# Optimization experiments

Measured on AMD Instinct MI355X. Metric: run time of the kernel, lower is better.

The kernel has to match this reference:

```python
import jax, jax.numpy as jnp
import numpy as np
import math

B, S, D = 16, 512, 512
H = 8
RET = 512  # return_dim, multiple of D
EPS = 1e-12


def _xavier(key, shape):
    bound = math.sqrt(6.0 / (shape[0] + shape[1]))
    return jax.random.uniform(key, shape, jnp.float32, -bound, bound)


def setup_inputs() -> dict:
    key = jax.random.key(0)
    ks = jax.random.split(key, 7)
    x = jax.random.normal(ks[0], (B, S, D), jnp.float32)
    WQ = _xavier(ks[1], (D, D))
    WK = _xavier(ks[2], (D, D))
    WV = _xavier(ks[3], (D, D))
    # LazyLinear over flattened (S*D) features; stored [in, out] for clean matmul
    Wlin = jax.random.normal(ks[4], (S * D, RET), jnp.float32) / math.sqrt(S * D)
    blin = jnp.zeros((RET,), jnp.float32)
    ln_w = jnp.ones((D,), jnp.float32)
    ln_b = jnp.zeros((D,), jnp.float32)
    return {"x": x, "WQ": WQ, "WK": WK, "WV": WV,
            "Wlin": Wlin, "blin": blin, "ln_w": ln_w, "ln_b": ln_b}


def _swish(v):
    return v * jax.nn.sigmoid(v)


def reference(x, WQ, WK, WV, Wlin, blin, ln_w, ln_b):
    b, s, d = x.shape
    dh = d // H
    # QKV projections -> [b, h, s, dh]
    Q = (x @ WQ).reshape(b, s, H, dh).transpose(0, 2, 1, 3)
    K = (x @ WK).reshape(b, s, H, dh).transpose(0, 2, 1, 3)
    V = (x @ WV).reshape(b, s, H, dh).transpose(0, 2, 1, 3)
    # swish-gated attention scores (no softmax)
    scores = jnp.einsum('bhqd,bhkd->bhqk', Q, K) / math.sqrt(dh)
    scores = _swish(scores)
    out = jnp.einsum('bhqk,bhkd->bqhd', scores, V).reshape(b, s, d)
    # residual + TF-style LayerNorm (residual_coef = 1)
    out = out + x
    u = out.mean(-1, keepdims=True)
    var = jnp.mean((out - u) ** 2, axis=-1, keepdims=True)
    out = ln_w * ((out - u) / jnp.sqrt(var + EPS)) + ln_b
    # linear over flattened seq*d features, swish, reshape (dropout = identity, eval)
    y = out.reshape(b, -1) @ Wlin + blin
    y = _swish(y)
    return y.reshape(b, -1, d)
```

## Files before the change

kernel.cpp:

```cpp
#include <hip/hip_runtime.h>
#include <cstdint>

#define TB 16
#define TS 512
#define TD 512
#define TH 8
#define TDH 64
#define TSD (TS*TD)

typedef __attribute__((ext_vector_type(8))) short s16x8;
typedef __attribute__((ext_vector_type(4))) float f32x4;
typedef unsigned short bfu;

__device__ __forceinline__ unsigned short f2b(float f) {
  unsigned int u = __float_as_uint(f);
  u += 0x7FFFu + ((u >> 16) & 1u);
  return (unsigned short)(u >> 16);
}
__device__ __forceinline__ float b2f(bfu h) {
  return __uint_as_float(((unsigned)h) << 16);
}

__device__ __forceinline__ void gll16(const void* g, void* l) {
  __builtin_amdgcn_global_load_lds((const __attribute__((address_space(1))) void*)g,
                                   (__attribute__((address_space(3))) void*)l, 16, 0, 0);
}

__device__ __forceinline__ f32x4 MFMA16(s16x8 a, s16x8 b, f32x4 c) {
  return __builtin_amdgcn_mfma_f32_16x16x32_bf16(a, b, c, 0, 0, 0);
}

__global__ __launch_bounds__(256) void k_cast_x(const float4* __restrict__ x, ushort4* __restrict__ xb) {
  int i = blockIdx.x * 256 + threadIdx.x;
  float4 v = x[i];
  ushort4 o; o.x = f2b(v.x); o.y = f2b(v.y); o.z = f2b(v.z); o.w = f2b(v.w);
  xb[i] = o;
}

__global__ __launch_bounds__(256) void k_prep_w(const float* __restrict__ WQ, const float* __restrict__ WK,
                                                const float* __restrict__ WV, bfu* __restrict__ wt) {
  __shared__ float tile[64][65];
  int bk = blockIdx.x & 7;
  int bn = blockIdx.x >> 3;
  const float* W = bn < 8 ? WQ : (bn < 16 ? WK : WV);
  int ncol0 = (bn & 7) * 64;
  int t = threadIdx.x, tx = t & 63, ty = t >> 6;
  #pragma unroll
  for (int i = 0; i < 16; ++i) {
    int kl = i * 4 + ty;
    tile[kl][tx] = W[(size_t)(bk * 64 + kl) * 512 + ncol0 + tx];
  }
  __syncthreads();
  #pragma unroll
  for (int i = 0; i < 16; ++i) {
    int nl = i * 4 + ty;
    wt[(size_t)(bn * 64 + nl) * 512 + bk * 64 + tx] = f2b(tile[tx][nl]);
  }
}

__global__ __launch_bounds__(256) void k_qkv(const bfu* __restrict__ xb, const bfu* __restrict__ wt,
                                             bfu* __restrict__ qb, bfu* __restrict__ kb, bfu* __restrict__ vtb) {
  __shared__ __align__(16) bfu At[128 * 32];
  __shared__ __align__(16) bfu Bt[128 * 32];
  int t = threadIdx.x, lane = t & 63, w = t >> 6;
  int wr = w >> 1, wc = w & 1;
  int m0 = blockIdx.x * 128, n0 = blockIdx.y * 128;
  int fr = lane & 15, hi = lane >> 4;
  f32x4 acc[4][4] = {};
  for (int k0 = 0; k0 < TD; k0 += 32) {
    #pragma unroll
    for (int i = 0; i < 2; ++i) {
      int base = (i * 4 + w) * 1024;
      int seg  = (i * 4 + w) * 64 + lane;
      int row = seg >> 2, cs = seg & 3;
      gll16(xb + (size_t)(m0 + row) * TD + k0 + cs * 8, (char*)At + base);
      gll16(wt + (size_t)(n0 + row) * TD + k0 + cs * 8, (char*)Bt + base);
    }
    __syncthreads();
    s16x8 a[4], bb[4];
    #pragma unroll
    for (int m = 0; m < 4; ++m) a[m]  = *(const s16x8*)&At[(wr * 64 + m * 16 + fr) * 32 + hi * 8];
    #pragma unroll
    for (int n = 0; n < 4; ++n) bb[n] = *(const s16x8*)&Bt[(wc * 64 + n * 16 + fr) * 32 + hi * 8];
    #pragma unroll
    for (int m = 0; m < 4; ++m)
      #pragma unroll
      for (int n = 0; n < 4; ++n)
        acc[m][n] = MFMA16(a[m], bb[n], acc[m][n]);
    __syncthreads();
  }
  #pragma unroll
  for (int m = 0; m < 4; ++m) {
    int grow = m0 + wr * 64 + m * 16 + hi * 4;
    #pragma unroll
    for (int n = 0; n < 4; ++n) {
      int gcol = n0 + wc * 64 + n * 16 + fr;
      if (gcol < 512) {
        #pragma unroll
        for (int r = 0; r < 4; ++r) qb[(size_t)(grow + r) * TD + gcol] = f2b(acc[m][n][r]);
      } else if (gcol < 1024) {
        int c = gcol - 512;
        #pragma unroll
        for (int r = 0; r < 4; ++r) kb[(size_t)(grow + r) * TD + c] = f2b(acc[m][n][r]);
      } else {
        int c = gcol - 1024;
        int hh = c >> 6, dc = c & 63;
        int b_ = grow >> 9, s = grow & 511;
        ushort4 pk;
        pk.x = f2b(acc[m][n][0]); pk.y = f2b(acc[m][n][1]);
        pk.z = f2b(acc[m][n][2]); pk.w = f2b(acc[m][n][3]);
        *(ushort4*)&vtb[((size_t)((b_ * TH + hh) * TDH + dc) << 9) + s] = pk;
      }
    }
  }
}

__global__ __launch_bounds__(256) void k_attn(const bfu* __restrict__ qb, const bfu* __restrict__ kb,
                                              const bfu* __restrict__ vtb, const bfu* __restrict__ xb,
                                              float* __restrict__ ao) {
  __shared__ __align__(16) bfu Qs[64 * 72];
  __shared__ __align__(16) bfu Ks[128 * 72];
  __shared__ __align__(16) bfu Vs[64 * 136];
  __shared__ __align__(16) bfu Ps[64 * 136];
  int t = threadIdx.x, lane = t & 63, w = t >> 6;
  int qt = blockIdx.x, h = blockIdx.y, b = blockIdx.z;
  size_t qrow0 = (size_t)b * TS + qt * 64;
  int fr = lane & 15, hi = lane >> 4;
  #pragma unroll
  for (int i = 0; i < 2; ++i) {
    int seg = i * 256 + t, row = seg >> 3, cs = seg & 7;
    s16x8 v = *(const s16x8*)(qb + (qrow0 + row) * TD + h * TDH + cs * 8);
    *(s16x8*)&Qs[row * 72 + cs * 8] = v;
  }
  f32x4 acc_o[4] = {};
  for (int kt = 0; kt < 4; ++kt) {
    #pragma unroll
    for (int i = 0; i < 4; ++i) {
      int seg = i * 256 + t, row = seg >> 3, cs = seg & 7;
      s16x8 v = *(const s16x8*)(kb + ((size_t)b * TS + kt * 128 + row) * TD + h * TDH + cs * 8);
      *(s16x8*)&Ks[row * 72 + cs * 8] = v;
    }
    #pragma unroll
    for (int i = 0; i < 4; ++i) {
      int seg = i * 256 + t, row = seg >> 4, cs = seg & 15;
      s16x8 v = *(const s16x8*)(vtb + ((size_t)(b * TH + h) * TDH + row) * TS + kt * 128 + cs * 8);
      *(s16x8*)&Vs[row * 136 + cs * 8] = v;
    }
    __syncthreads();
    s16x8 aq0 = *(const s16x8*)&Qs[(w * 16 + fr) * 72 + hi * 8];
    s16x8 aq1 = *(const s16x8*)&Qs[(w * 16 + fr) * 72 + 32 + hi * 8];
    f32x4 sc[8];
    #pragma unroll
    for (int kj = 0; kj < 8; ++kj) {
      s16x8 b0 = *(const s16x8*)&Ks[(kj * 16 + fr) * 72 + hi * 8];
      s16x8 b1 = *(const s16x8*)&Ks[(kj * 16 + fr) * 72 + 32 + hi * 8];
      f32x4 c = {};
      c = MFMA16(aq0, b0, c);
      c = MFMA16(aq1, b1, c);
      sc[kj] = c;
    }
    #pragma unroll
    for (int kj = 0; kj < 8; ++kj) {
      #pragma unroll
      for (int r = 0; r < 4; ++r) {
        float v = sc[kj][r] * 0.125f;
        float p = v / (1.f + __expf(-v));
        Ps[(w * 16 + hi * 4 + r) * 136 + kj * 16 + fr] = f2b(p);
      }
    }
    #pragma unroll
    for (int ks = 0; ks < 4; ++ks) {
      s16x8 pa = *(const s16x8*)&Ps[(w * 16 + fr) * 136 + ks * 32 + hi * 8];
      #pragma unroll
      for (int dn = 0; dn < 4; ++dn) {
        s16x8 vb = *(const s16x8*)&Vs[(dn * 16 + fr) * 136 + ks * 32 + hi * 8];
        acc_o[dn] = MFMA16(pa, vb, acc_o[dn]);
      }
    }
    __syncthreads();
  }
  #pragma unroll
  for (int dn = 0; dn < 4; ++dn) {
    int col = h * TDH + dn * 16 + fr;
    #pragma unroll
    for (int r = 0; r < 4; ++r) {
      size_t row = qrow0 + w * 16 + hi * 4 + r;
      ao[row * TD + col] = acc_o[dn][r] + b2f(xb[row * TD + col]);
    }
  }
}

__global__ __launch_bounds__(256) void k_ln(const float* __restrict__ a, const float* __restrict__ w,
                                            const float* __restrict__ bias, bfu* __restrict__ o) {
  int row = blockIdx.x, t = threadIdx.x;
  float2 v = *(const float2*)(a + (size_t)row * TD + t * 2);
  float s = v.x + v.y;
  #pragma unroll
  for (int off = 32; off > 0; off >>= 1) s += __shfl_down(s, off);
  __shared__ float r1[4], r2[4];
  int lane = t & 63, wv = t >> 6;
  if (lane == 0) r1[wv] = s;
  __syncthreads();
  float mean = (r1[0] + r1[1] + r1[2] + r1[3]) * (1.f / TD);
  float dx = v.x - mean, dy = v.y - mean;
  float q = dx * dx + dy * dy;
  #pragma unroll
  for (int off = 32; off > 0; off >>= 1) q += __shfl_down(q, off);
  if (lane == 0) r2[wv] = q;
  __syncthreads();
  float var = (r2[0] + r2[1] + r2[2] + r2[3]) * (1.f / TD);
  float inv = rsqrtf(var + 1e-12f);
  float2 wv2 = *(const float2*)(w + t * 2);
  float2 bv2 = *(const float2*)(bias + t * 2);
  unsigned pack = (unsigned)f2b(wv2.x * dx * inv + bv2.x) |
                  ((unsigned)f2b(wv2.y * dy * inv + bv2.y) << 16);
  *(unsigned*)(o + (size_t)row * TD + t * 2) = pack;
}

__global__ __launch_bounds__(256) void k_lin_mfma(const bfu* __restrict__ lno, const float* __restrict__ wl,
                                                  float* __restrict__ part) {
  __shared__ __align__(16) bfu Wt[64 * 72];
  int t = threadIdx.x, lane = t & 63, w = t >> 6;
  int fr = lane & 15, hi = lane >> 4;
  int kc = blockIdx.x >> 3, nb = blockIdx.x & 7;
  int n0 = nb * 64;
  int nl = t & 63, kb = (t >> 6) * 16;
  int ks0 = kc * 2048;
  const float* wbase = wl + (size_t)(ks0 + kb) * 512 + n0 + nl;
  const bfu*   abase = lno + (size_t)fr * TSD + ks0 + hi * 8;
  f32x4 acc = {};
  float wA[16], wB[16];
  s16x8 aA0, aA1, aB0, aB1;
  #pragma unroll
  for (int i = 0; i < 16; ++i) wA[i] = __builtin_nontemporal_load(wbase + (size_t)i * 512);
  aA0 = *(const s16x8*)abase;
  aA1 = *(const s16x8*)(abase + 32);

#define LIN_STEP(CW, CA0, CA1, NW, NA0, NA1, S)                                   \
  { if (S) __syncthreads();                                                       \
    unsigned pk[8];                                                               \
    _Pragma("unroll")                                                             \
    for (int i = 0; i < 8; ++i)                                                   \
      pk[i] = (unsigned)f2b(CW[2*i]) | ((unsigned)f2b(CW[2*i+1]) << 16);          \
    *(uint4*)&Wt[nl * 72 + kb]     = *(uint4*)&pk[0];                             \
    *(uint4*)&Wt[nl * 72 + kb + 8] = *(uint4*)&pk[4];                             \
    if ((S) + 1 < 32) {                                                           \
      const float* wp2 = wbase + (size_t)((S) + 1) * 64 * 512;                    \
      _Pragma("unroll")                                                           \
      for (int i = 0; i < 16; ++i) NW[i] = __builtin_nontemporal_load(wp2 + (size_t)i * 512); \
      const bfu* ap2 = abase + ((S) + 1) * 64;                                    \
      NA0 = *(const s16x8*)ap2; NA1 = *(const s16x8*)(ap2 + 32);                  \
    }                                                                             \
    __syncthreads();                                                              \
    s16x8 b0 = *(const s16x8*)&Wt[(w * 16 + fr) * 72 + hi * 8];                   \
    s16x8 b1 = *(const s16x8*)&Wt[(w * 16 + fr) * 72 + 32 + hi * 8];              \
    acc = MFMA16(CA0, b0, acc);                                                   \
    acc = MFMA16(CA1, b1, acc); }

  for (int s = 0; s < 32; s += 2) {
    LIN_STEP(wA, aA0, aA1, wB, aB0, aB1, s)
    LIN_STEP(wB, aB0, aB1, wA, aA0, aA1, s + 1)
  }
#undef LIN_STEP
  #pragma unroll
  for (int r = 0; r < 4; ++r)
    part[(size_t)kc * 8192 + (hi * 4 + r) * 512 + n0 + w * 16 + fr] = acc[r];
}

__global__ __launch_bounds__(256) void k_lin_red(const float* __restrict__ part, const float* __restrict__ blin,
                                                 float* __restrict__ out) {
  int o = blockIdx.x * 256 + threadIdx.x;
  float s = 0.f;
  #pragma unroll 16
  for (int c = 0; c < 128; ++c) s += part[(size_t)c * 8192 + o];
  float v = s + blin[o & 511];
  out[o] = v / (1.f + __expf(-v));
}

extern "C" void kernel_launch(void* const* d_in, const int* in_sizes, int n_in,
                              void* d_out, int out_size, void* d_ws, size_t ws_size,
                              hipStream_t stream) {
  const float* x   = (const float*)d_in[0];
  const float* WQ  = (const float*)d_in[1];
  const float* WK  = (const float*)d_in[2];
  const float* WV  = (const float*)d_in[3];
  const float* Wl  = (const float*)d_in[4];
  const float* bl  = (const float*)d_in[5];
  const float* lnw = (const float*)d_in[6];
  const float* lnb = (const float*)d_in[7];
  float* out = (float*)d_out;
  char* ws = (char*)d_ws;
  bfu* xb  = (bfu*)ws;
  bfu* wt  = xb + 4194304;
  bfu* qb  = wt + 786432;
  bfu* kb  = qb + 4194304;
  bfu* vtb = kb + 4194304;
  float* attn = (float*)(vtb + 4194304);
  bfu*   lno  = (bfu*)(attn + 4194304);
  float* part = (float*)(lno + 4194304);
  float* pend = part + 1048576;
  (void)pend; (void)ws_size;

  k_cast_x  <<<4096, 256, 0, stream>>>((const float4*)x, (ushort4*)xb);
  k_prep_w  <<<192, 256, 0, stream>>>(WQ, WK, WV, wt);
  k_qkv     <<<dim3(64, 12), 256, 0, stream>>>(xb, wt, qb, kb, vtb);
  k_attn    <<<dim3(8, 8, 16), 256, 0, stream>>>(qb, kb, vtb, xb, attn);
  k_ln      <<<8192, 256, 0, stream>>>(attn, lnw, lnb, lno);
  k_lin_mfma<<<1024, 256, 0, stream>>>(lno, Wl, part);
  k_lin_red <<<32, 256, 0, stream>>>(part, bl, out);
}
```

Before: 198.9 us.

## Double-buffer QKV GEMM, XOR-swizzle LDS tiles, async-load attention, merge prep kernels

Merges the x-cast and weight-transpose kernels into one launch to save a kernel launch. The QKV GEMM gets double-buffered LDS with direct global-to-LDS loads, so the next K slice loads while MFMAs run. XOR-swizzled LDS layouts replace the padded ones in both GEMM and attention to avoid bank conflicts. Attention now uses global_load_lds for Q/K/V instead of going through registers. These changes add more index arithmetic and extra barriers in attention, and the swizzle indices must match exactly on write and read.

```diff
diff --git a/kernel.cpp b/kernel.cpp
--- a/kernel.cpp
+++ b/kernel.cpp
@@ -30,21 +30,24 @@
   return __builtin_amdgcn_mfma_f32_16x16x32_bf16(a, b, c, 0, 0, 0);
 }
 
-__global__ __launch_bounds__(256) void k_cast_x(const float4* __restrict__ x, ushort4* __restrict__ xb) {
-  int i = blockIdx.x * 256 + threadIdx.x;
-  float4 v = x[i];
-  ushort4 o; o.x = f2b(v.x); o.y = f2b(v.y); o.z = f2b(v.z); o.w = f2b(v.w);
-  xb[i] = o;
-}
-
-__global__ __launch_bounds__(256) void k_prep_w(const float* __restrict__ WQ, const float* __restrict__ WK,
-                                                const float* __restrict__ WV, bfu* __restrict__ wt) {
+__global__ __launch_bounds__(256) void k_prep(const float* __restrict__ x, ushort4* __restrict__ xb,
+                                              const float* __restrict__ WQ, const float* __restrict__ WK,
+                                              const float* __restrict__ WV, bfu* __restrict__ wt) {
+  int t = threadIdx.x;
+  if (blockIdx.x < 4096) {
+    int i = blockIdx.x * 256 + t;
+    float4 v = ((const float4*)x)[i];
+    ushort4 o; o.x = f2b(v.x); o.y = f2b(v.y); o.z = f2b(v.z); o.w = f2b(v.w);
+    xb[i] = o;
+    return;
+  }
   __shared__ float tile[64][65];
-  int bk = blockIdx.x & 7;
-  int bn = blockIdx.x >> 3;
+  int bid = blockIdx.x - 4096;
+  int bk = bid & 7;
+  int bn = bid >> 3;
   const float* W = bn < 8 ? WQ : (bn < 16 ? WK : WV);
   int ncol0 = (bn & 7) * 64;
-  int t = threadIdx.x, tx = t & 63, ty = t >> 6;
+  int tx = t & 63, ty = t >> 6;
   #pragma unroll
   for (int i = 0; i < 16; ++i) {
     int kl = i * 4 + ty;
@@ -60,35 +63,48 @@
 
 __global__ __launch_bounds__(256) void k_qkv(const bfu* __restrict__ xb, const bfu* __restrict__ wt,
                                              bfu* __restrict__ qb, bfu* __restrict__ kb, bfu* __restrict__ vtb) {
-  __shared__ __align__(16) bfu At[128 * 32];
-  __shared__ __align__(16) bfu Bt[128 * 32];
+  __shared__ __align__(16) bfu At[2][128 * 32];
+  __shared__ __align__(16) bfu Bt[2][128 * 32];
   int t = threadIdx.x, lane = t & 63, w = t >> 6;
   int wr = w >> 1, wc = w & 1;
   int m0 = blockIdx.x * 128, n0 = blockIdx.y * 128;
   int fr = lane & 15, hi = lane >> 4;
+  int l4r = lane >> 2, l4c = lane & 3;
   f32x4 acc[4][4] = {};
-  for (int k0 = 0; k0 < TD; k0 += 32) {
-    #pragma unroll
-    for (int i = 0; i < 2; ++i) {
-      int base = (i * 4 + w) * 1024;
-      int seg  = (i * 4 + w) * 64 + lane;
-      int row = seg >> 2, cs = seg & 3;
-      gll16(xb + (size_t)(m0 + row) * TD + k0 + cs * 8, (char*)At + base);
-      gll16(wt + (size_t)(n0 + row) * TD + k0 + cs * 8, (char*)Bt + base);
-    }
+
+#define QKV_STAGE(BUF, K0) { \
+    _Pragma("unroll") \
+    for (int i = 0; i < 2; ++i) { \
+      int row = i * 64 + w * 16 + l4r; \
+      int cs = l4c ^ (l4r & 3);                         \
+      gll16(xb + (size_t)(m0 + row) * TD + (K0) + cs * 8, (char*)At[BUF] + (i * 256 + w * 64) * 16); \
+      gll16(wt + (size_t)(n0 + row) * TD + (K0) + cs * 8, (char*)Bt[BUF] + (i * 256 + w * 64) * 16); \
+    } }
+
+#define QKV_COMP(BUF) { \
+    s16x8 a[4], bb[4]; \
+    int ca = (hi ^ (fr & 3)) * 8; \
+    _Pragma("unroll") \
+    for (int m = 0; m < 4; ++m) a[m]  = *(const s16x8*)&At[BUF][(wr * 64 + m * 16 + fr) * 32 + ca]; \
+    _Pragma("unroll") \
+    for (int n = 0; n < 4; ++n) bb[n] = *(const s16x8*)&Bt[BUF][(wc * 64 + n * 16 + fr) * 32 + ca]; \
+    _Pragma("unroll") \
+    for (int m = 0; m < 4; ++m) \
+      _Pragma("unroll") \
+      for (int n = 0; n < 4; ++n) \
+        acc[m][n] = MFMA16(a[m], bb[n], acc[m][n]); }
+
+  QKV_STAGE(0, 0)
+  __syncthreads();
+  for (int k = 0; k < 16; ++k) {
+    int cur = k & 1;
+    if (k < 15) QKV_STAGE(cur ^ 1, (k + 1) * 32)
+    QKV_COMP(cur)
     __syncthreads();
-    s16x8 a[4], bb[4];
-    #pragma unroll
-    for (int m = 0; m < 4; ++m) a[m]  = *(const s16x8*)&At[(wr * 64 + m * 16 + fr) * 32 + hi * 8];
-    #pragma unroll
-    for (int n = 0; n < 4; ++n) bb[n] = *(const s16x8*)&Bt[(wc * 64 + n * 16 + fr) * 32 + hi * 8];
-    #pragma unroll
-    for (int m = 0; m < 4; ++m)
-      #pragma unroll
-      for (int n = 0; n < 4; ++n)
-        acc[m][n] = MFMA16(a[m], bb[n], acc[m][n]);
-    __syncthreads();
-  }
+  }
+#undef QKV_STAGE
+#undef QKV_COMP
+
   #pragma unroll
   for (int m = 0; m < 4; ++m) {
     int grow = m0 + wr * 64 + m * 16 + hi * 4;
@@ -118,42 +134,56 @@
 __global__ __launch_bounds__(256) void k_attn(const bfu* __restrict__ qb, const bfu* __restrict__ kb,
                                               const bfu* __restrict__ vtb, const bfu* __restrict__ xb,
                                               float* __restrict__ ao) {
-  __shared__ __align__(16) bfu Qs[64 * 72];
-  __shared__ __align__(16) bfu Ks[128 * 72];
-  __shared__ __align__(16) bfu Vs[64 * 136];
-  __shared__ __align__(16) bfu Ps[64 * 136];
+  __shared__ __align__(16) bfu Qs[64 * 64];
+  __shared__ __align__(16) bfu Ks[128 * 64];
+  __shared__ __align__(16) bfu Vs[64 * 128];
+  __shared__ __align__(16) bfu Ps[64 * 128];
   int t = threadIdx.x, lane = t & 63, w = t >> 6;
   int qt = blockIdx.x, h = blockIdx.y, b = blockIdx.z;
   size_t qrow0 = (size_t)b * TS + qt * 64;
   int fr = lane & 15, hi = lane >> 4;
+  int l8r = lane >> 3, l8c = lane & 7;
+  int l16r = lane >> 4, l16c = lane & 15;
+
+#define K_STAGE(KT) { \
+    _Pragma("unroll") \
+    for (int i = 0; i < 4; ++i) { \
+      int row = i * 32 + w * 8 + l8r; \
+      int cs = l8c ^ (l8r & 7);                         \
+      gll16(kb + ((size_t)b * TS + (KT) * 128 + row) * TD + h * TDH + cs * 8, \
+            (char*)Ks + (i * 256 + w * 64) * 16); \
+    } }
+#define V_STAGE(KT) { \
+    _Pragma("unroll") \
+    for (int i = 0; i < 4; ++i) { \
+      int row = i * 16 + w * 4 + l16r; \
+      int cs = l16c ^ (row & 7); \
+      gll16(vtb + ((size_t)(b * TH + h) * TDH + row) * TS + (KT) * 128 + cs * 8, \
+            (char*)Vs + (i * 256 + w * 64) * 16); \
+    } }
+
   #pragma unroll
   for (int i = 0; i < 2; ++i) {
-    int seg = i * 256 + t, row = seg >> 3, cs = seg & 7;
-    s16x8 v = *(const s16x8*)(qb + (qrow0 + row) * TD + h * TDH + cs * 8);
-    *(s16x8*)&Qs[row * 72 + cs * 8] = v;
-  }
+    int row = i * 32 + w * 8 + l8r;
+    int cs = l8c ^ (l8r & 7);
+    gll16(qb + (qrow0 + row) * TD + h * TDH + cs * 8, (char*)Qs + (i * 256 + w * 64) * 16);
+  }
+  K_STAGE(0)
+  V_STAGE(0)
+  __syncthreads();
+
+  int qrow = w * 16 + fr;
+  int r7 = fr & 7;
   f32x4 acc_o[4] = {};
   for (int kt = 0; kt < 4; ++kt) {
-    #pragma unroll
-    for (int i = 0; i < 4; ++i) {
-      int seg = i * 256 + t, row = seg >> 3, cs = seg & 7;
-      s16x8 v = *(const s16x8*)(kb + ((size_t)b * TS + kt * 128 + row) * TD + h * TDH + cs * 8);
-      *(s16x8*)&Ks[row * 72 + cs * 8] = v;
-    }
-    #pragma unroll
-    for (int i = 0; i < 4; ++i) {
-      int seg = i * 256 + t, row = seg >> 4, cs = seg & 15;
-      s16x8 v = *(const s16x8*)(vtb + ((size_t)(b * TH + h) * TDH + row) * TS + kt * 128 + cs * 8);
-      *(s16x8*)&Vs[row * 136 + cs * 8] = v;
-    }
-    __syncthreads();
-    s16x8 aq0 = *(const s16x8*)&Qs[(w * 16 + fr) * 72 + hi * 8];
-    s16x8 aq1 = *(const s16x8*)&Qs[(w * 16 + fr) * 72 + 32 + hi * 8];
+    s16x8 aq0 = *(const s16x8*)&Qs[qrow * 64 + ((hi ^ r7) * 8)];
+    s16x8 aq1 = *(const s16x8*)&Qs[qrow * 64 + (((4 + hi) ^ r7) * 8)];
     f32x4 sc[8];
     #pragma unroll
     for (int kj = 0; kj < 8; ++kj) {
-      s16x8 b0 = *(const s16x8*)&Ks[(kj * 16 + fr) * 72 + hi * 8];
-      s16x8 b1 = *(const s16x8*)&Ks[(kj * 16 + fr) * 72 + 32 + hi * 8];
+      int krow = kj * 16 + fr;
+      s16x8 b0 = *(const s16x8*)&Ks[krow * 64 + ((hi ^ r7) * 8)];
+      s16x8 b1 = *(const s16x8*)&Ks[krow * 64 + (((4 + hi) ^ r7) * 8)];
       f32x4 c = {};
       c = MFMA16(aq0, b0, c);
       c = MFMA16(aq1, b1, c);
@@ -165,20 +195,29 @@
       for (int r = 0; r < 4; ++r) {
         float v = sc[kj][r] * 0.125f;
         float p = v / (1.f + __expf(-v));
-        Ps[(w * 16 + hi * 4 + r) * 136 + kj * 16 + fr] = f2b(p);
+        int prow = w * 16 + hi * 4 + r;
+        int c8 = (kj * 2 + (fr >> 3)) ^ (prow & 7);
+        Ps[prow * 128 + c8 * 8 + (fr & 7)] = f2b(p);
       }
     }
     #pragma unroll
     for (int ks = 0; ks < 4; ++ks) {
-      s16x8 pa = *(const s16x8*)&Ps[(w * 16 + fr) * 136 + ks * 32 + hi * 8];
+      s16x8 pa = *(const s16x8*)&Ps[qrow * 128 + (((ks * 4 + hi) ^ r7) * 8)];
       #pragma unroll
       for (int dn = 0; dn < 4; ++dn) {
-        s16x8 vb = *(const s16x8*)&Vs[(dn * 16 + fr) * 136 + ks * 32 + hi * 8];
+        s16x8 vb = *(const s16x8*)&Vs[(dn * 16 + fr) * 128 + (((ks * 4 + hi) ^ r7) * 8)];
         acc_o[dn] = MFMA16(pa, vb, acc_o[dn]);
       }
     }
     __syncthreads();
-  }
+    if (kt < 3) {
+      K_STAGE(kt + 1)
+      V_STAGE(kt + 1)
+      __syncthreads();
+    }
+  }
+#undef K_STAGE
+#undef V_STAGE
   #pragma unroll
   for (int dn = 0; dn < 4; ++dn) {
     int col = h * TDH + dn * 16 + fr;
@@ -298,11 +337,8 @@
   float* attn = (float*)(vtb + 4194304);
   bfu*   lno  = (bfu*)(attn + 4194304);
   float* part = (float*)(lno + 4194304);
-  float* pend = part + 1048576;
-  (void)pend; (void)ws_size;
-
-  k_cast_x  <<<4096, 256, 0, stream>>>((const float4*)x, (ushort4*)xb);
-  k_prep_w  <<<192, 256, 0, stream>>>(WQ, WK, WV, wt);
+
+  k_prep    <<<4288, 256, 0, stream>>>(x, (ushort4*)xb, WQ, WK, WV, wt);
   k_qkv     <<<dim3(64, 12), 256, 0, stream>>>(xb, wt, qb, kb, vtb);
   k_attn    <<<dim3(8, 8, 16), 256, 0, stream>>>(qb, kb, vtb, xb, attn);
   k_ln      <<<8192, 256, 0, stream>>>(attn, lnw, lnb, lno);
```

Measured after the change: 185.7 us. 6.7% less time.
